# Kernel optimization log

Measured on AMD Instinct MI355X. Metric: run time of the kernel, lower is better.

## Reference

```python
import jax, jax.numpy as jnp
import numpy as np

N = 50000          # nodes
E = 1_600_000      # edges
IN = 256           # in_channels
C = 32             # hidden_channels (per-head width)
HEADS = 4
BN_EPS = 1e-5


def setup_inputs() -> dict:
    key = jax.random.key(0)
    ks = jax.random.split(key, 32)
    g = lambda k, shp, s=0.1: (jax.random.normal(k, shp, jnp.float32) * s)
    inp = {
        "x": jax.random.normal(ks[0], (N, IN), jnp.float32),
        "edge_index": jax.random.randint(ks[1], (2, E), 0, N, jnp.int64),
        "edge_attr": jax.random.uniform(ks[2], (E, 1), jnp.float32),
        # conv1 (GATConv in=IN, out=C, heads=HEADS, edge_dim=1)
        "W1": g(ks[3], (IN, HEADS * C)),
        "as1": g(ks[4], (HEADS, C)),
        "ad1": g(ks[5], (HEADS, C)),
        "We1": g(ks[6], (1, HEADS * C)),
        "ae1": g(ks[7], (HEADS, C)),
        "b1": jnp.zeros((HEADS * C,), jnp.float32),
        # bn1 (eval mode, running_mean=0, running_var=1)
        "g1": jnp.ones((HEADS * C,), jnp.float32),
        "be1": jnp.zeros((HEADS * C,), jnp.float32),
        # conv2 (GATConv in=HEADS*C, out=C, heads=1, concat=False, edge_dim=1)
        "W2": g(ks[8], (HEADS * C, C)),
        "as2": g(ks[9], (1, C)),
        "ad2": g(ks[10], (1, C)),
        "We2": g(ks[11], (1, C)),
        "ae2": g(ks[12], (1, C)),
        "b2": jnp.zeros((C,), jnp.float32),
        # bn2
        "g2": jnp.ones((C,), jnp.float32),
        "be2": jnp.zeros((C,), jnp.float32),
        # classifier: Linear(C,16) -> ReLU -> Linear(16,2)
        "Wc1": g(ks[13], (C, 16)),
        "bc1": jnp.zeros((16,), jnp.float32),
        "Wc2": g(ks[14], (16, 2)),
        "bc2": jnp.zeros((2,), jnp.float32),
        "Wr1": g(ks[15], (C, 16)),
        "br1": jnp.zeros((16,), jnp.float32),
        "Wr2": g(ks[16], (16, 1)),
        "br2": jnp.zeros((1,), jnp.float32),
    }
    return inp


def _gat_conv(x, src, dst, eattr, W, a_src, a_dst, We, a_e, bias, heads, c, concat):
    n = x.shape[0]
    xs = (x @ W).reshape(n, heads, c)                       # [N,H,C]
    al_s = (xs * a_src).sum(-1)                              # [N,H]
    al_d = (xs * a_dst).sum(-1)                              # [N,H]
    ee = (eattr @ We).reshape(-1, heads, c)                  # [E,H,C]
    al_e = (ee * a_e).sum(-1)                                # [E,H]
    alpha = al_s[src] + al_d[dst] + al_e                     # [E,H]
    alpha = jax.nn.leaky_relu(alpha, 0.2)
    # segment softmax over destination node
    mx = jax.ops.segment_max(alpha, dst, num_segments=n)
    ex = jnp.exp(alpha - mx[dst])
    den = jax.ops.segment_sum(ex, dst, num_segments=n)
    a = ex / (den[dst] + 1e-16)                              # [E,H]
    out = jax.ops.segment_sum(xs[src] * a[..., None], dst, num_segments=n)  # [N,H,C]
    out = out.reshape(n, heads * c) if concat else out.mean(axis=1)
    return out + bias


def _add_self_loops(src, dst, eattr, n):
    loop = jnp.arange(n, dtype=src.dtype)
    fill = jnp.broadcast_to(eattr.mean(axis=0, keepdims=True), (n, eattr.shape[1]))
    return (jnp.concatenate([src, loop]), jnp.concatenate([dst, loop]),
            jnp.concatenate([eattr, fill], axis=0))


def _bn_eval(x, gamma, beta):
    # running_mean=0, running_var=1 (fresh BatchNorm1d, eval mode)
    return x * (gamma / jnp.sqrt(1.0 + BN_EPS)) + beta


def reference(x, edge_index, edge_attr, W1, as1, ad1, We1, ae1, b1, g1, be1,
              W2, as2, ad2, We2, ae2, b2, g2, be2,
              Wc1, bc1, Wc2, bc2, Wr1, br1, Wr2, br2):
    n = x.shape[0]
    src, dst, ea = _add_self_loops(edge_index[0], edge_index[1], edge_attr, n)
    h = _gat_conv(x, src, dst, ea, W1, as1, ad1, We1, ae1, b1, HEADS, C, True)
    h = jax.nn.elu(_bn_eval(h, g1, be1))
    h = _gat_conv(h, src, dst, ea, W2, as2, ad2, We2, ae2, b2, 1, C, False)
    h = jax.nn.elu(_bn_eval(h, g2, be2))
    cls = jax.nn.relu(h @ Wc1 + bc1) @ Wc2 + bc2             # [N,2]
    reg = (jax.nn.relu(h @ Wr1 + br1) @ Wr2 + br2)[:, 0]     # [N]
    return cls, reg, h
```

## Files before the change

kernel.cpp:

```cpp
#include <hip/hip_runtime.h>
#include <cstdint>
#include <cstddef>

#define NN 50000
#define EE 1600000
#define IN_DIM 256
#define HC 128
#define CD 32
#define BN_RS 0.9999950000374997f

#define CAP1 120
#define CAP2 128
#define NBKT 196
#define S1_B 782
#define HIST_B 320
#define G1_B 782

typedef __attribute__((ext_vector_type(8))) short short8;
typedef __attribute__((ext_vector_type(4))) float f32x4;

__device__ __forceinline__ float lrelu(float a) { return a > 0.f ? a : 0.2f * a; }
__device__ __forceinline__ float elu(float a) { return a > 0.f ? a : (__expf(a) - 1.f); }

__device__ __forceinline__ unsigned short f2bf(float f) {
    unsigned int u = __float_as_uint(f);
    unsigned int r = (u + 0x7FFFu + ((u >> 16) & 1u)) >> 16;
    return (unsigned short)r;
}
__device__ __forceinline__ float bf2f(unsigned short b) {
    return __uint_as_float(((unsigned int)b) << 16);
}
__device__ __forceinline__ float2 bf2f2(unsigned int p) {
    float2 r;
    r.x = __uint_as_float(p << 16);
    r.y = __uint_as_float(p & 0xFFFF0000u);
    return r;
}
__device__ __forceinline__ void unpack_edge(unsigned long long p, int& s, float& eav) {
    s = (int)(unsigned int)(p & 0xFFFFFFFFull);
    eav = __uint_as_float((unsigned int)(p >> 32));
}
__device__ __forceinline__ float pick4(float a, float b, float c, float d, int h) {
    return (h & 2) ? ((h & 1) ? d : c) : ((h & 1) ? b : a);
}

__device__ __forceinline__ int block_excl_scan_256(int v, int tid, int* wsum) {
    int lane = tid & 63, wv = tid >> 6;
    int x = v;
    #pragma unroll
    for (int off = 1; off < 64; off <<= 1) {
        int y = __shfl_up(x, off);
        if (lane >= off) x += y;
    }
    if (lane == 63) wsum[wv] = x;
    __syncthreads();
    int wpre = 0;
    #pragma unroll
    for (int w = 0; w < 4; w++)
        if (w < wv) wpre += wsum[w];
    return wpre + x - v;
}

__global__ __launch_bounds__(256) void k0_prep(const float* __restrict__ W1,
                                               const float* __restrict__ W2,
                                               const float* __restrict__ We1,
                                               const float* __restrict__ ae1,
                                               const float* __restrict__ We2,
                                               const float* __restrict__ ae2,
                                               unsigned short* __restrict__ W1hi,
                                               unsigned short* __restrict__ W1lo,
                                               unsigned short* __restrict__ W2hi,
                                               unsigned short* __restrict__ W2lo,
                                               float* __restrict__ consts,
                                               int* __restrict__ bucketHist) {
    int blk = blockIdx.x;
    int tid = threadIdx.x;
    if (blk < 16) {
        int t = blk * 256 + tid;
        int lane = t & 63;
        int kt = (t >> 6) & 7;
        int nt = t >> 9;
        int kbase = kt * 32 + (lane >> 4) * 8;
        int col = nt * 16 + (lane & 15);
        size_t obase = (size_t)t * 8;
        #pragma unroll
        for (int j = 0; j < 8; j++) {
            float w = W1[(size_t)(kbase + j) * HC + col];
            unsigned short h = f2bf(w);
            W1hi[obase + j] = h;
            W1lo[obase + j] = f2bf(w - bf2f(h));
        }
    } else if (blk < 18) {
        int t = (blk - 16) * 256 + tid;
        int lane = t & 63;
        int kt = (t >> 6) & 3;
        int nt = t >> 8;
        int kbase = kt * 32 + (lane >> 4) * 8;
        int col = nt * 16 + (lane & 15);
        size_t obase = (size_t)t * 8;
        #pragma unroll
        for (int j = 0; j < 8; j++) {
            float w = W2[(size_t)(kbase + j) * CD + col];
            unsigned short h = f2bf(w);
            W2hi[obase + j] = h;
            W2lo[obase + j] = f2bf(w - bf2f(h));
        }
    } else {
        if (tid < NBKT) bucketHist[tid] = 0;
        if (tid == 200) consts[0] = 0.f;
        if (tid < 4) {
            float s = 0.f;
            for (int c = 0; c < 32; c++) s += We1[tid * 32 + c] * ae1[tid * 32 + c];
            consts[2 + tid] = s;
        } else if (tid == 4) {
            float s = 0.f;
            for (int c = 0; c < 32; c++) s += We2[c] * ae2[c];
            consts[6] = s;
        }
    }
}

__global__ __launch_bounds__(256) void kA_hist_gemm1(const int* __restrict__ ei,
                                                     const float* __restrict__ ea,
                                                     const float* __restrict__ x,
                                                     const unsigned short* __restrict__ Whi,
                                                     const unsigned short* __restrict__ Wlo,
                                                     int* __restrict__ bucketHist,
                                                     float* __restrict__ easum,
                                                     unsigned short* __restrict__ xs1b) {
    __shared__ int h[256];
    int tid = threadIdx.x;
    if (blockIdx.x < HIST_B) {
        h[tid] = 0;
        __syncthreads();
        float s = 0.f;
        for (int i = blockIdx.x * 256 + tid; i < EE; i += HIST_B * 256) {
            atomicAdd(&h[ei[EE + i] >> 8], 1);
            s += ea[i];
        }
        __syncthreads();
        if (tid < NBKT && h[tid] > 0) atomicAdd(&bucketHist[tid], h[tid]);
        #pragma unroll
        for (int off = 32; off > 0; off >>= 1) s += __shfl_xor(s, off);
        if ((tid & 63) == 0) atomicAdd(easum, s);
    } else {
        int lane = tid & 63, wv = tid >> 6;
        int row0 = (blockIdx.x - HIST_B) * 64 + wv * 16;
        if (row0 >= NN) return;
        int m = lane & 15;
        int q = lane >> 4;
        f32x4 acc[8];
        #pragma unroll
        for (int nt = 0; nt < 8; nt++) acc[nt] = {0.f, 0.f, 0.f, 0.f};
        const float* xrow = x + (size_t)(row0 + m) * IN_DIM + q * 8;
        #pragma unroll
        for (int kt = 0; kt < 8; kt++) {
            float4 v0 = *(const float4*)(xrow + kt * 32);
            float4 v1 = *(const float4*)(xrow + kt * 32 + 4);
            float vv[8] = {v0.x, v0.y, v0.z, v0.w, v1.x, v1.y, v1.z, v1.w};
            short8 ahi, alo;
            #pragma unroll
            for (int j = 0; j < 8; j++) {
                unsigned short hh = f2bf(vv[j]);
                ahi[j] = (short)hh;
                alo[j] = (short)f2bf(vv[j] - bf2f(hh));
            }
            #pragma unroll
            for (int nt = 0; nt < 8; nt++) {
                size_t fb = ((size_t)(nt * 8 + kt) * 64 + lane) * 8;
                short8 bhi = *(const short8*)(Whi + fb);
                short8 blo = *(const short8*)(Wlo + fb);
                acc[nt] = __builtin_amdgcn_mfma_f32_16x16x32_bf16(ahi, bhi, acc[nt], 0, 0, 0);
                acc[nt] = __builtin_amdgcn_mfma_f32_16x16x32_bf16(ahi, blo, acc[nt], 0, 0, 0);
                acc[nt] = __builtin_amdgcn_mfma_f32_16x16x32_bf16(alo, bhi, acc[nt], 0, 0, 0);
            }
        }
        #pragma unroll
        for (int nt = 0; nt < 8; nt++) {
            #pragma unroll
            for (int reg = 0; reg < 4; reg++) {
                int row = row0 + q * 4 + reg;
                xs1b[(size_t)row * HC + nt * 16 + m] = f2bf(acc[nt][reg]);
            }
        }
    }
}

__global__ void bucket_scan(const int* __restrict__ bucketHist,
                            int* __restrict__ bucketBase,
                            int* __restrict__ bucketCursor,
                            int* __restrict__ indptr,
                            float* __restrict__ consts) {
    __shared__ int wsum[4];
    int tid = threadIdx.x;
    int v = (tid < NBKT) ? bucketHist[tid] : 0;
    int excl = block_excl_scan_256(v, tid, wsum);
    if (tid <= NBKT) bucketBase[tid] = (tid == NBKT) ? EE : excl;
    if (tid < NBKT) bucketCursor[tid] = excl;
    if (tid == 0) { indptr[NN] = EE; consts[1] = consts[0] / (float)EE; }
}

__global__ __launch_bounds__(256) void kB_stage1_al1(const int* __restrict__ ei,
                                                     const float* __restrict__ ea,
                                                     int* __restrict__ bucketCursor,
                                                     uint2* __restrict__ Apack,
                                                     const unsigned short* __restrict__ xs1b,
                                                     const float* __restrict__ as1,
                                                     const float* __restrict__ ad1,
                                                     float* __restrict__ als,
                                                     float* __restrict__ ald) {
    __shared__ int cnt[256];
    __shared__ int basel[256];
    __shared__ int gbase[256];
    __shared__ int wsum[4];
    __shared__ int sdst[2048];
    __shared__ int ssrc[2048];
    __shared__ float sea[2048];
    int tid = threadIdx.x;
    if (blockIdx.x < S1_B) {
        int base = blockIdx.x * 2048;
        cnt[tid] = 0;
        __syncthreads();
        int d[8], s[8], r[8], bk[8];
        float e[8];
        #pragma unroll
        for (int k = 0; k < 8; k++) {
            int i = base + k * 256 + tid;
            if (i < EE) {
                d[k] = ei[EE + i];
                s[k] = ei[i];
                e[k] = ea[i];
                bk[k] = d[k] >> 8;
                r[k] = atomicAdd(&cnt[bk[k]], 1);
            } else d[k] = -1;
        }
        __syncthreads();
        int v = cnt[tid];
        int excl = block_excl_scan_256(v, tid, wsum);
        basel[tid] = excl;
        if (tid < NBKT) gbase[tid] = atomicAdd(&bucketCursor[tid], v);
        __syncthreads();
        #pragma unroll
        for (int k = 0; k < 8; k++) {
            if (d[k] >= 0) {
                int slot = basel[bk[k]] + r[k];
                sdst[slot] = d[k];
                ssrc[slot] = s[k];
                sea[slot] = e[k];
            }
        }
        __syncthreads();
        int total = basel[255] + cnt[255];
        for (int slot = tid; slot < total; slot += 256) {
            int dd = sdst[slot];
            int b = dd >> 8;
            int pos = gbase[b] + (slot - basel[b]);
            Apack[pos] = make_uint2((unsigned int)ssrc[slot] | ((unsigned int)(dd & 255) << 24),
                                    __float_as_uint(sea[slot]));
        }
    } else {
        int t = (blockIdx.x - S1_B) * 256 + tid;
        if (t < NN * 4) {
            int hh = t & 3;
            const unsigned int* xp = (const unsigned int*)(xs1b + (size_t)t * 32);
            const float* ap = as1 + hh * 32;
            const float* dp = ad1 + hh * 32;
            float s = 0.f, d = 0.f;
            #pragma unroll
            for (int q = 0; q < 16; q++) {
                float2 v = bf2f2(xp[q]);
                s += v.x * ap[q * 2] + v.y * ap[q * 2 + 1];
                d += v.x * dp[q * 2] + v.y * dp[q * 2 + 1];
            }
            als[t] = s;
            ald[t] = d;
        }
    }
}

__global__ __launch_bounds__(1024) void stage2_kernel(const int* __restrict__ bucketBase,
                                                      const uint2* __restrict__ Apack,
                                                      int* __restrict__ indptr,
                                                      unsigned long long* __restrict__ edgedat) {
    __shared__ int cnt[256];
    __shared__ int dbase[256];
    int tid = threadIdx.x;
    int b = blockIdx.x;
    int start = bucketBase[b], end = bucketBase[b + 1];
    if (tid < 256) cnt[tid] = 0;
    __syncthreads();
    for (int i = start + tid; i < end; i += 1024) atomicAdd(&cnt[Apack[i].x >> 24], 1);
    __syncthreads();
    if (tid < 64) {
        int b4 = tid * 4;
        int c0 = cnt[b4], c1 = cnt[b4 + 1], c2 = cnt[b4 + 2], c3 = cnt[b4 + 3];
        int t = c0 + c1 + c2 + c3;
        int x = t;
        #pragma unroll
        for (int off = 1; off < 64; off <<= 1) {
            int y = __shfl_up(x, off);
            if (tid >= off) x += y;
        }
        int e0 = x - t;
        dbase[b4] = e0;
        dbase[b4 + 1] = e0 + c0;
        dbase[b4 + 2] = e0 + c0 + c1;
        dbase[b4 + 3] = e0 + c0 + c1 + c2;
    }
    __syncthreads();
    if (tid < 256) {
        int n = b * 256 + tid;
        if (n < NN) indptr[n] = start + dbase[tid];
        cnt[tid] = 0;
    }
    __syncthreads();
    for (int i = start + tid; i < end; i += 1024) {
        uint2 p = Apack[i];
        int dl = p.x >> 24;
        int r = atomicAdd(&cnt[dl], 1);
        int pos = start + dbase[dl] + r;
        edgedat[pos] = (unsigned long long)(p.x & 0xFFFFFFu) |
                       ((unsigned long long)p.y << 32);
    }
}

#define ACC4(vv, ww) { float2 p0_ = bf2f2((vv).x); float2 p1_ = bf2f2((vv).y); \
    acc0 += p0_.x * (ww); acc1 += p0_.y * (ww); acc2 += p1_.x * (ww); acc3 += p1_.y * (ww); }

__global__ __launch_bounds__(256, 8) void gat1_agg(
    const unsigned short* __restrict__ xs1b, const float* __restrict__ als,
    const float* __restrict__ ald, const unsigned long long* __restrict__ edgedat,
    const int* __restrict__ indptr, const float* __restrict__ consts,
    const float* __restrict__ b1, const float* __restrict__ g1,
    const float* __restrict__ be1,
    unsigned short* __restrict__ h1hi, unsigned short* __restrict__ h1lo) {
    __shared__ __align__(16) float exbuf[8][CAP1][4];
    __shared__ int srcbuf[8][CAP1];
    int tid = threadIdx.x;
    int l = tid & 31;
    int nb = tid >> 5;
    int n = blockIdx.x * 8 + nb;
    int start = indptr[n];
    int deg = indptr[n + 1] - start;
    float ea_mean = consts[1];
    float ce0 = consts[2], ce1 = consts[3], ce2 = consts[4], ce3 = consts[5];
    float4 a4d = *(const float4*)(ald + (size_t)n * 4);
    float4 a4s = *(const float4*)(als + (size_t)n * 4);
    float ex00 = __expf(lrelu(a4s.x + a4d.x + ea_mean * ce0));
    float ex01 = __expf(lrelu(a4s.y + a4d.y + ea_mean * ce1));
    float ex02 = __expf(lrelu(a4s.z + a4d.z + ea_mean * ce2));
    float ex03 = __expf(lrelu(a4s.w + a4d.w + ea_mean * ce3));
    float sm0 = 0.f, sm1 = 0.f, sm2 = 0.f, sm3 = 0.f;
    const unsigned long long* edp = edgedat + start;
    for (int i = l; i < deg; i += 32) {
        int s; float eav;
        unpack_edge(edp[i], s, eav);
        float4 v4 = *(const float4*)(als + (size_t)s * 4);
        float4 ex4;
        ex4.x = __expf(lrelu(v4.x + a4d.x + eav * ce0)); sm0 += ex4.x;
        ex4.y = __expf(lrelu(v4.y + a4d.y + eav * ce1)); sm1 += ex4.y;
        ex4.z = __expf(lrelu(v4.z + a4d.z + eav * ce2)); sm2 += ex4.z;
        ex4.w = __expf(lrelu(v4.w + a4d.w + eav * ce3)); sm3 += ex4.w;
        if (i < CAP1) {
            srcbuf[nb][i] = s * (HC * 2);
            *(float4*)(&exbuf[nb][i][0]) = ex4;
        }
    }
    #pragma unroll
    for (int off = 16; off > 0; off >>= 1) {
        sm0 += __shfl_xor(sm0, off);
        sm1 += __shfl_xor(sm1, off);
        sm2 += __shfl_xor(sm2, off);
        sm3 += __shfl_xor(sm3, off);
    }
    int h2 = l >> 3;
    float ex0sel = pick4(ex00, ex01, ex02, ex03, h2);
    float inv = 1.0f / (pick4(sm0, sm1, sm2, sm3, h2) + ex0sel + 1e-16f);
    int mcap = deg < CAP1 ? deg : CAP1;
    const char* xb = (const char*)xs1b + (size_t)l * 8;
    float acc0, acc1, acc2, acc3;
    {
        uint2 v = *(const uint2*)(xb + (size_t)n * (HC * 2));
        float2 p0 = bf2f2(v.x), p1 = bf2f2(v.y);
        acc0 = p0.x * ex0sel; acc1 = p0.y * ex0sel;
        acc2 = p1.x * ex0sel; acc3 = p1.y * ex0sel;
    }
    int i = 0;
    for (; i + 8 <= mcap; i += 8) {
        int o0 = srcbuf[nb][i + 0], o1 = srcbuf[nb][i + 1];
        int o2 = srcbuf[nb][i + 2], o3 = srcbuf[nb][i + 3];
        int o4 = srcbuf[nb][i + 4], o5 = srcbuf[nb][i + 5];
        int o6 = srcbuf[nb][i + 6], o7 = srcbuf[nb][i + 7];
        float w0 = exbuf[nb][i + 0][h2], w1 = exbuf[nb][i + 1][h2];
        float w2 = exbuf[nb][i + 2][h2], w3 = exbuf[nb][i + 3][h2];
        float w4 = exbuf[nb][i + 4][h2], w5 = exbuf[nb][i + 5][h2];
        float w6 = exbuf[nb][i + 6][h2], w7 = exbuf[nb][i + 7][h2];
        uint2 v0 = *(const uint2*)(xb + o0);
        uint2 v1 = *(const uint2*)(xb + o1);
        uint2 v2 = *(const uint2*)(xb + o2);
        uint2 v3 = *(const uint2*)(xb + o3);
        uint2 v4 = *(const uint2*)(xb + o4);
        uint2 v5 = *(const uint2*)(xb + o5);
        uint2 v6 = *(const uint2*)(xb + o6);
        uint2 v7 = *(const uint2*)(xb + o7);
        ACC4(v0, w0); ACC4(v1, w1); ACC4(v2, w2); ACC4(v3, w3);
        ACC4(v4, w4); ACC4(v5, w5); ACC4(v6, w6); ACC4(v7, w7);
    }
    for (; i < mcap; i++) {
        int o = srcbuf[nb][i];
        float w = exbuf[nb][i][h2];
        uint2 v = *(const uint2*)(xb + o);
        ACC4(v, w);
    }
    if (deg > CAP1) {
        float aldsel = pick4(a4d.x, a4d.y, a4d.z, a4d.w, h2);
        float cesel = pick4(ce0, ce1, ce2, ce3, h2);
        for (int j = CAP1; j < deg; j++) {
            int s; float eav;
            unpack_edge(edp[j], s, eav);
            float w = __expf(lrelu(als[(size_t)s * 4 + h2] + aldsel + eav * cesel));
            uint2 v = *(const uint2*)(xb + (size_t)s * (HC * 2));
            ACC4(v, w);
        }
    }
    acc0 *= inv; acc1 *= inv; acc2 *= inv; acc3 *= inv;
    int c = l * 4;
    float4 bb = *(const float4*)(b1 + c);
    float4 gg = *(const float4*)(g1 + c);
    float4 eb = *(const float4*)(be1 + c);
    float o0 = elu((acc0 + bb.x) * (gg.x * BN_RS) + eb.x);
    float o1 = elu((acc1 + bb.y) * (gg.y * BN_RS) + eb.y);
    float o2 = elu((acc2 + bb.z) * (gg.z * BN_RS) + eb.z);
    float o3 = elu((acc3 + bb.w) * (gg.w * BN_RS) + eb.w);
    unsigned short h0 = f2bf(o0), h1v = f2bf(o1), h2v = f2bf(o2), h3v = f2bf(o3);
    unsigned short l0 = f2bf(o0 - bf2f(h0)), l1 = f2bf(o1 - bf2f(h1v));
    unsigned short l2 = f2bf(o2 - bf2f(h2v)), l3 = f2bf(o3 - bf2f(h3v));
    uint2 hiw, low;
    hiw.x = (unsigned int)h0 | ((unsigned int)h1v << 16);
    hiw.y = (unsigned int)h2v | ((unsigned int)h3v << 16);
    low.x = (unsigned int)l0 | ((unsigned int)l1 << 16);
    low.y = (unsigned int)l2 | ((unsigned int)l3 << 16);
    *(uint2*)(h1hi + (size_t)n * HC + c) = hiw;
    *(uint2*)(h1lo + (size_t)n * HC + c) = low;
}

__global__ __launch_bounds__(256) void gemm2_mfma(const unsigned short* __restrict__ h1hi,
                                                  const unsigned short* __restrict__ h1lo,
                                                  const unsigned short* __restrict__ W2hi,
                                                  const unsigned short* __restrict__ W2lo,
                                                  const float* __restrict__ as2,
                                                  const float* __restrict__ ad2,
                                                  unsigned short* __restrict__ xs2b,
                                                  float* __restrict__ als2,
                                                  float* __restrict__ ald2) {
    int tid = threadIdx.x;
    int lane = tid & 63, wv = tid >> 6;
    int row0 = blockIdx.x * 64 + wv * 16;
    if (row0 >= NN) return;
    int m = lane & 15, q = lane >> 4;
    f32x4 acc[2];
    acc[0] = {0.f, 0.f, 0.f, 0.f};
    acc[1] = {0.f, 0.f, 0.f, 0.f};
    const unsigned short* rhi = h1hi + (size_t)(row0 + m) * HC + q * 8;
    const unsigned short* rlo = h1lo + (size_t)(row0 + m) * HC + q * 8;
    #pragma unroll
    for (int kt = 0; kt < 4; kt++) {
        short8 ahi = *(const short8*)(rhi + kt * 32);
        short8 alo = *(const short8*)(rlo + kt * 32);
        #pragma unroll
        for (int nt = 0; nt < 2; nt++) {
            size_t fb = ((size_t)(nt * 4 + kt) * 64 + lane) * 8;
            short8 bhi = *(const short8*)(W2hi + fb);
            short8 blo = *(const short8*)(W2lo + fb);
            acc[nt] = __builtin_amdgcn_mfma_f32_16x16x32_bf16(ahi, bhi, acc[nt], 0, 0, 0);
            acc[nt] = __builtin_amdgcn_mfma_f32_16x16x32_bf16(ahi, blo, acc[nt], 0, 0, 0);
            acc[nt] = __builtin_amdgcn_mfma_f32_16x16x32_bf16(alo, bhi, acc[nt], 0, 0, 0);
        }
    }
    float a0 = as2[m], a1 = as2[m + 16];
    float d0 = ad2[m], d1 = ad2[m + 16];
    #pragma unroll
    for (int reg = 0; reg < 4; reg++) {
        int row = row0 + q * 4 + reg;
        xs2b[(size_t)row * CD + m]      = f2bf(acc[0][reg]);
        xs2b[(size_t)row * CD + 16 + m] = f2bf(acc[1][reg]);
        float s = acc[0][reg] * a0 + acc[1][reg] * a1;
        float d = acc[0][reg] * d0 + acc[1][reg] * d1;
        #pragma unroll
        for (int off = 1; off < 16; off <<= 1) {
            s += __shfl_xor(s, off);
            d += __shfl_xor(d, off);
        }
        if (m == 0) { als2[row] = s; ald2[row] = d; }
    }
}

__global__ __launch_bounds__(256) void gat2_agg(
    const unsigned short* __restrict__ xs2b, const float* __restrict__ als,
    const float* __restrict__ ald, const unsigned long long* __restrict__ edgedat,
    const int* __restrict__ indptr, const float* __restrict__ consts,
    const float* __restrict__ b2, const float* __restrict__ g2, const float* __restrict__ be2,
    const float* __restrict__ Wc1, const float* __restrict__ bc1,
    const float* __restrict__ Wc2, const float* __restrict__ bc2,
    const float* __restrict__ Wr1, const float* __restrict__ br1,
    const float* __restrict__ Wr2, const float* __restrict__ br2,
    float* __restrict__ hout, float* __restrict__ cls, float* __restrict__ reg) {
    __shared__ float exbuf[4][CAP2];
    __shared__ int srcbuf[4][CAP2];
    __shared__ __align__(16) float hbuf[4][32];
    int wv = threadIdx.x >> 6;
    int lane = threadIdx.x & 63;
    int n = blockIdx.x * 4 + wv;
    int start = indptr[n];
    int deg = indptr[n + 1] - start;
    float ea_mean = consts[1];
    float ce = consts[6];
    float aldn = ald[n];
    float ex0 = __expf(lrelu(als[n] + aldn + ea_mean * ce));
    float sm = 0.f;
    const unsigned long long* edp = edgedat + start;
    for (int i = lane; i < deg; i += 64) {
        int s; float eav;
        unpack_edge(edp[i], s, eav);
        float exv = __expf(lrelu(als[s] + aldn + eav * ce));
        if (i < CAP2) { srcbuf[wv][i] = s * (CD * 2); exbuf[wv][i] = exv; }
        sm += exv;
    }
    #pragma unroll
    for (int off = 32; off > 0; off >>= 1) sm += __shfl_xor(sm, off);
    float invd = 1.0f / (sm + ex0 + 1e-16f);
    int mcap = deg < CAP2 ? deg : CAP2;
    int oct = lane >> 3, lo = lane & 7;
    const char* xb = (const char*)xs2b + (size_t)lo * 8;
    float acc0 = 0.f, acc1 = 0.f, acc2 = 0.f, acc3 = 0.f;
    if (oct == 0) {
        uint2 v = *(const uint2*)(xb + (size_t)n * (CD * 2));
        float2 p0 = bf2f2(v.x), p1 = bf2f2(v.y);
        acc0 = p0.x * ex0; acc1 = p0.y * ex0; acc2 = p1.x * ex0; acc3 = p1.y * ex0;
    }
    for (int i = oct; i < mcap; i += 8) {
        float w = exbuf[wv][i];
        int o = srcbuf[wv][i];
        uint2 v = *(const uint2*)(xb + o);
        ACC4(v, w);
    }
    for (int i = CAP2 + oct; i < deg; i += 8) {
        int s; float eav;
        unpack_edge(edp[i], s, eav);
        float w = __expf(lrelu(als[s] + aldn + eav * ce));
        uint2 v = *(const uint2*)(xb + (size_t)s * (CD * 2));
        ACC4(v, w);
    }
    #pragma unroll
    for (int off = 8; off < 64; off <<= 1) {
        acc0 += __shfl_xor(acc0, off);
        acc1 += __shfl_xor(acc1, off);
        acc2 += __shfl_xor(acc2, off);
        acc3 += __shfl_xor(acc3, off);
    }
    if (lane < 8) {
        int c = lo * 4;
        float4 bb = *(const float4*)(b2 + c);
        float4 gg = *(const float4*)(g2 + c);
        float4 eb = *(const float4*)(be2 + c);
        float o0 = elu((acc0 * invd + bb.x) * (gg.x * BN_RS) + eb.x);
        float o1 = elu((acc1 * invd + bb.y) * (gg.y * BN_RS) + eb.y);
        float o2 = elu((acc2 * invd + bb.z) * (gg.z * BN_RS) + eb.z);
        float o3 = elu((acc3 * invd + bb.w) * (gg.w * BN_RS) + eb.w);
        *(float4*)(&hbuf[wv][c]) = make_float4(o0, o1, o2, o3);
        *(float4*)(hout + (size_t)n * CD + c) = make_float4(o0, o1, o2, o3);
    }
    float r0 = 0.f, r1 = 0.f;
    if (lane < 32) {
        int j = lane & 15;
        bool iscls = lane < 16;
        float s = iscls ? bc1[j] : br1[j];
        #pragma unroll
        for (int cc = 0; cc < 32; cc++) {
            float w = iscls ? Wc1[cc * 16 + j] : Wr1[cc * 16 + j];
            s += hbuf[wv][cc] * w;
        }
        s = fmaxf(s, 0.f);
        if (iscls) { r0 = s * Wc2[j * 2]; r1 = s * Wc2[j * 2 + 1]; }
        else       { r0 = s * Wr2[j]; }
    }
    #pragma unroll
    for (int off = 1; off < 16; off <<= 1) {
        r0 += __shfl_xor(r0, off);
        r1 += __shfl_xor(r1, off);
    }
    if (lane == 0)  *(float2*)(cls + (size_t)n * 2) = make_float2(r0 + bc2[0], r1 + bc2[1]);
    if (lane == 16) reg[n] = r0 + br2[0];
}

extern "C" void kernel_launch(void* const* d_in, const int* in_sizes, int n_in,
                              void* d_out, int out_size, void* d_ws, size_t ws_size,
                              hipStream_t stream) {
    const float* x   = (const float*)d_in[0];
    const int*   ei  = (const int*)d_in[1];
    const float* ea  = (const float*)d_in[2];
    const float* W1  = (const float*)d_in[3];
    const float* as1 = (const float*)d_in[4];
    const float* ad1 = (const float*)d_in[5];
    const float* We1 = (const float*)d_in[6];
    const float* ae1 = (const float*)d_in[7];
    const float* b1  = (const float*)d_in[8];
    const float* g1  = (const float*)d_in[9];
    const float* be1 = (const float*)d_in[10];
    const float* W2  = (const float*)d_in[11];
    const float* as2 = (const float*)d_in[12];
    const float* ad2 = (const float*)d_in[13];
    const float* We2 = (const float*)d_in[14];
    const float* ae2 = (const float*)d_in[15];
    const float* b2  = (const float*)d_in[16];
    const float* g2  = (const float*)d_in[17];
    const float* be2 = (const float*)d_in[18];
    const float* Wc1 = (const float*)d_in[19];
    const float* bc1 = (const float*)d_in[20];
    const float* Wc2 = (const float*)d_in[21];
    const float* bc2 = (const float*)d_in[22];
    const float* Wr1 = (const float*)d_in[23];
    const float* br1 = (const float*)d_in[24];
    const float* Wr2 = (const float*)d_in[25];
    const float* br2 = (const float*)d_in[26];

    char* ws = (char*)d_ws;
    unsigned short* xs1b = (unsigned short*)(ws + 0);
    unsigned short* h1hi = (unsigned short*)(ws + 12800000);
    unsigned short* h1lo = (unsigned short*)(ws + 25600000);
    uint2* Apack         = (uint2*)(ws + 12800000);
    unsigned short* xs2b = (unsigned short*)(ws + 38400000);
    float* als1          = (float*)(ws + 41600000);
    float* ald1          = (float*)(ws + 42400000);
    float* als2          = (float*)(ws + 43200000);
    float* ald2          = (float*)(ws + 43400000);
    float* consts        = (float*)(ws + 43600000);
    int*   bucketHist    = (int*)(ws + 43600128);
    int*   bucketBase    = (int*)(ws + 43601024);
    int*   bucketCursor  = (int*)(ws + 43601920);
    int*   indptr        = (int*)(ws + 43602816);
    unsigned long long* edgedat = (unsigned long long*)(ws + 43802824);
    unsigned short* W1hi = (unsigned short*)(ws + 56602832);
    unsigned short* W1lo = (unsigned short*)(ws + 56668368);
    unsigned short* W2hi = (unsigned short*)(ws + 56733904);
    unsigned short* W2lo = (unsigned short*)(ws + 56742096);

    float* out_cls = (float*)d_out;
    float* out_reg = out_cls + 2 * NN;
    float* out_h   = out_cls + 3 * NN;

    k0_prep<<<19, 256, 0, stream>>>(W1, W2, We1, ae1, We2, ae2,
                                    W1hi, W1lo, W2hi, W2lo, consts, bucketHist);
    kA_hist_gemm1<<<HIST_B + G1_B, 256, 0, stream>>>(ei, ea, x, W1hi, W1lo,
                                                     bucketHist, consts, xs1b);
    bucket_scan<<<1, 256, 0, stream>>>(bucketHist, bucketBase, bucketCursor, indptr, consts);
    kB_stage1_al1<<<S1_B + 782, 256, 0, stream>>>(ei, ea, bucketCursor, Apack,
                                                  xs1b, as1, ad1, als1, ald1);
    stage2_kernel<<<NBKT, 1024, 0, stream>>>(bucketBase, Apack, indptr, edgedat);

    gat1_agg<<<NN / 8, 256, 0, stream>>>(xs1b, als1, ald1, edgedat, indptr, consts,
                                         b1, g1, be1, h1hi, h1lo);
    gemm2_mfma<<<G1_B, 256, 0, stream>>>(h1hi, h1lo, W2hi, W2lo, as2, ad2,
                                         xs2b, als2, ald2);
    gat2_agg<<<NN / 4, 256, 0, stream>>>(xs2b, als2, ald2, edgedat, indptr, consts,
                                         b2, g2, be2, Wc1, bc1, Wc2, bc2,
                                         Wr1, br1, Wr2, br2, out_h, out_cls, out_reg);
}
```

Before: 332.3 us.

## Fuse layer-2 projection GEMM into GAT1 aggregation epilogue via shared memory

The layer-1 aggregation kernel now writes its normalized bf16 hi/lo output rows to shared memory, and one wavefront per block runs the W2 MFMA projection plus the als2/ald2 reductions for those 8 nodes. This removes the global write and re-read of the 128-wide h1 hi/lo arrays and one kernel launch. Each 16-row MFMA tile now covers only 8 real rows, so half the MFMA work is duplicated, and the other wavefronts sit idle after the barrier. CAP1 is cut from 120 to 96 to make room in shared memory for the staging buffers, which also changes the per-node edge cache capacity.

```diff
diff --git a/kernel.cpp b/kernel.cpp
--- a/kernel.cpp
+++ b/kernel.cpp
@@ -9,7 +9,7 @@
 #define CD 32
 #define BN_RS 0.9999950000374997f
 
-#define CAP1 120
+#define CAP1 96
 #define CAP2 128
 #define NBKT 196
 #define S1_B 782
@@ -327,15 +327,21 @@
 #define ACC4(vv, ww) { float2 p0_ = bf2f2((vv).x); float2 p1_ = bf2f2((vv).y); \
     acc0 += p0_.x * (ww); acc1 += p0_.y * (ww); acc2 += p1_.x * (ww); acc3 += p1_.y * (ww); }
 
-__global__ __launch_bounds__(256, 8) void gat1_agg(
+#define H1P 136
+__global__ __launch_bounds__(256, 8) void gat1_gemm2(
     const unsigned short* __restrict__ xs1b, const float* __restrict__ als,
     const float* __restrict__ ald, const unsigned long long* __restrict__ edgedat,
     const int* __restrict__ indptr, const float* __restrict__ consts,
     const float* __restrict__ b1, const float* __restrict__ g1,
     const float* __restrict__ be1,
-    unsigned short* __restrict__ h1hi, unsigned short* __restrict__ h1lo) {
+    const unsigned short* __restrict__ W2hi, const unsigned short* __restrict__ W2lo,
+    const float* __restrict__ as2, const float* __restrict__ ad2,
+    unsigned short* __restrict__ xs2b, float* __restrict__ als2,
+    float* __restrict__ ald2) {
     __shared__ __align__(16) float exbuf[8][CAP1][4];
     __shared__ int srcbuf[8][CAP1];
+    __shared__ __align__(16) unsigned short h1hi_s[8][H1P];
+    __shared__ __align__(16) unsigned short h1lo_s[8][H1P];
     int tid = threadIdx.x;
     int l = tid & 31;
     int nb = tid >> 5;
@@ -440,58 +446,52 @@
     hiw.y = (unsigned int)h2v | ((unsigned int)h3v << 16);
     low.x = (unsigned int)l0 | ((unsigned int)l1 << 16);
     low.y = (unsigned int)l2 | ((unsigned int)l3 << 16);
-    *(uint2*)(h1hi + (size_t)n * HC + c) = hiw;
-    *(uint2*)(h1lo + (size_t)n * HC + c) = low;
-}
-
-__global__ __launch_bounds__(256) void gemm2_mfma(const unsigned short* __restrict__ h1hi,
-                                                  const unsigned short* __restrict__ h1lo,
-                                                  const unsigned short* __restrict__ W2hi,
-                                                  const unsigned short* __restrict__ W2lo,
-                                                  const float* __restrict__ as2,
-                                                  const float* __restrict__ ad2,
-                                                  unsigned short* __restrict__ xs2b,
-                                                  float* __restrict__ als2,
-                                                  float* __restrict__ ald2) {
-    int tid = threadIdx.x;
-    int lane = tid & 63, wv = tid >> 6;
-    int row0 = blockIdx.x * 64 + wv * 16;
-    if (row0 >= NN) return;
+    *(uint2*)(&h1hi_s[nb][c]) = hiw;
+    *(uint2*)(&h1lo_s[nb][c]) = low;
+    __syncthreads();
+    if (tid >= 64) return;
+
+    int lane = tid;
     int m = lane & 15, q = lane >> 4;
-    f32x4 acc[2];
-    acc[0] = {0.f, 0.f, 0.f, 0.f};
-    acc[1] = {0.f, 0.f, 0.f, 0.f};
-    const unsigned short* rhi = h1hi + (size_t)(row0 + m) * HC + q * 8;
-    const unsigned short* rlo = h1lo + (size_t)(row0 + m) * HC + q * 8;
+    int r8 = m & 7;
+    f32x4 g2acc0 = {0.f, 0.f, 0.f, 0.f};
+    f32x4 g2acc1 = {0.f, 0.f, 0.f, 0.f};
     #pragma unroll
     for (int kt = 0; kt < 4; kt++) {
-        short8 ahi = *(const short8*)(rhi + kt * 32);
-        short8 alo = *(const short8*)(rlo + kt * 32);
-        #pragma unroll
-        for (int nt = 0; nt < 2; nt++) {
-            size_t fb = ((size_t)(nt * 4 + kt) * 64 + lane) * 8;
-            short8 bhi = *(const short8*)(W2hi + fb);
-            short8 blo = *(const short8*)(W2lo + fb);
-            acc[nt] = __builtin_amdgcn_mfma_f32_16x16x32_bf16(ahi, bhi, acc[nt], 0, 0, 0);
-            acc[nt] = __builtin_amdgcn_mfma_f32_16x16x32_bf16(ahi, blo, acc[nt], 0, 0, 0);
-            acc[nt] = __builtin_amdgcn_mfma_f32_16x16x32_bf16(alo, bhi, acc[nt], 0, 0, 0);
-        }
-    }
+        short8 ahi = *(const short8*)(&h1hi_s[r8][q * 8 + kt * 32]);
+        short8 alo = *(const short8*)(&h1lo_s[r8][q * 8 + kt * 32]);
+        size_t fb0 = ((size_t)kt * 64 + lane) * 8;
+        size_t fb1 = ((size_t)(4 + kt) * 64 + lane) * 8;
+        short8 bhi0 = *(const short8*)(W2hi + fb0);
+        short8 blo0 = *(const short8*)(W2lo + fb0);
+        short8 bhi1 = *(const short8*)(W2hi + fb1);
+        short8 blo1 = *(const short8*)(W2lo + fb1);
+        g2acc0 = __builtin_amdgcn_mfma_f32_16x16x32_bf16(ahi, bhi0, g2acc0, 0, 0, 0);
+        g2acc0 = __builtin_amdgcn_mfma_f32_16x16x32_bf16(ahi, blo0, g2acc0, 0, 0, 0);
+        g2acc0 = __builtin_amdgcn_mfma_f32_16x16x32_bf16(alo, bhi0, g2acc0, 0, 0, 0);
+        g2acc1 = __builtin_amdgcn_mfma_f32_16x16x32_bf16(ahi, bhi1, g2acc1, 0, 0, 0);
+        g2acc1 = __builtin_amdgcn_mfma_f32_16x16x32_bf16(ahi, blo1, g2acc1, 0, 0, 0);
+        g2acc1 = __builtin_amdgcn_mfma_f32_16x16x32_bf16(alo, bhi1, g2acc1, 0, 0, 0);
+    }
+    int n0 = blockIdx.x * 8;
     float a0 = as2[m], a1 = as2[m + 16];
     float d0 = ad2[m], d1 = ad2[m + 16];
     #pragma unroll
-    for (int reg = 0; reg < 4; reg++) {
-        int row = row0 + q * 4 + reg;
-        xs2b[(size_t)row * CD + m]      = f2bf(acc[0][reg]);
-        xs2b[(size_t)row * CD + 16 + m] = f2bf(acc[1][reg]);
-        float s = acc[0][reg] * a0 + acc[1][reg] * a1;
-        float d = acc[0][reg] * d0 + acc[1][reg] * d1;
+    for (int rg = 0; rg < 4; rg++) {
+        int rloc = q * 4 + rg;
+        float s = g2acc0[rg] * a0 + g2acc1[rg] * a1;
+        float d = g2acc0[rg] * d0 + g2acc1[rg] * d1;
         #pragma unroll
         for (int off = 1; off < 16; off <<= 1) {
             s += __shfl_xor(s, off);
             d += __shfl_xor(d, off);
         }
-        if (m == 0) { als2[row] = s; ald2[row] = d; }
+        if (rloc < 8) {
+            int row = n0 + rloc;
+            xs2b[(size_t)row * CD + m]      = f2bf(g2acc0[rg]);
+            xs2b[(size_t)row * CD + 16 + m] = f2bf(g2acc1[rg]);
+            if (m == 0) { als2[row] = s; ald2[row] = d; }
+        }
     }
 }
 
@@ -626,8 +626,6 @@
 
     char* ws = (char*)d_ws;
     unsigned short* xs1b = (unsigned short*)(ws + 0);
-    unsigned short* h1hi = (unsigned short*)(ws + 12800000);
-    unsigned short* h1lo = (unsigned short*)(ws + 25600000);
     uint2* Apack         = (uint2*)(ws + 12800000);
     unsigned short* xs2b = (unsigned short*)(ws + 38400000);
     float* als1          = (float*)(ws + 41600000);
@@ -658,10 +656,9 @@
                                                   xs1b, as1, ad1, als1, ald1);
     stage2_kernel<<<NBKT, 1024, 0, stream>>>(bucketBase, Apack, indptr, edgedat);
 
-    gat1_agg<<<NN / 8, 256, 0, stream>>>(xs1b, als1, ald1, edgedat, indptr, consts,
-                                         b1, g1, be1, h1hi, h1lo);
-    gemm2_mfma<<<G1_B, 256, 0, stream>>>(h1hi, h1lo, W2hi, W2lo, as2, ad2,
-                                         xs2b, als2, ald2);
+    gat1_gemm2<<<NN / 8, 256, 0, stream>>>(xs1b, als1, ald1, edgedat, indptr, consts,
+                                           b1, g1, be1, W2hi, W2lo, as2, ad2,
+                                           xs2b, als2, ald2);
     gat2_agg<<<NN / 4, 256, 0, stream>>>(xs2b, als2, ald2, edgedat, indptr, consts,
                                          b2, g2, be2, Wc1, bc1, Wc2, bc2,
                                          Wr1, br1, Wr2, br2, out_h, out_cls, out_reg);
```

Result: no change. 327.6 us (-1.4%).
